# Performance work log

Hardware: AMD Instinct MI355X
Metric: run time of the kernel (lower is better)

The kernel has to match this reference:

```python
import jax, jax.numpy as jnp
import numpy as np

B, T, D, H = 4, 2048, 1024, 16
DH = D // H

def setup_inputs() -> dict:
    key = jax.random.key(0)
    ks = jax.random.split(key, 8)
    scale = 1.0 / np.sqrt(D)
    return {
        "q": jax.random.normal(ks[0], (B, T, D), dtype=jnp.float32),
        "k": jax.random.normal(ks[1], (B, T, D), dtype=jnp.float32),
        "v": jax.random.normal(ks[2], (B, T, D), dtype=jnp.float32),
        "wq": jax.random.normal(ks[3], (D, D), dtype=jnp.float32) * scale,
        "wk": jax.random.normal(ks[4], (D, D), dtype=jnp.float32) * scale,
        "wv": jax.random.normal(ks[5], (D, D), dtype=jnp.float32) * scale,
        "wo": jax.random.normal(ks[6], (D, D), dtype=jnp.float32) * scale,
        "mask": jnp.tril(jnp.ones((T, T), dtype=bool)),  # causal [Tq,Tk]
    }

def reference(q, k, v, wq, wk, wv, wo, mask):
    Bq, Tq, C = q.shape
    Tk = k.shape[1]
    # nn.Linear(bias=False): y = x @ W.T, W is [out,in]
    qh = (q @ wq.T).reshape(Bq, Tq, H, DH).transpose(0, 2, 1, 3)  # [B,H,Tq,DH]
    kh = (k @ wk.T).reshape(Bq, Tk, H, DH).transpose(0, 2, 1, 3)
    vh = (v @ wv.T).reshape(Bq, Tk, H, DH).transpose(0, 2, 1, 3)
    att = jnp.einsum("bhqd,bhkd->bhqk", qh, kh) / np.sqrt(DH)
    att = jnp.where(mask[None, None, :, :], att, -jnp.inf)
    att = jax.nn.softmax(att, axis=-1)
    out = jnp.einsum("bhqk,bhkd->bhqd", att, vh)
    out = out.transpose(0, 2, 1, 3).reshape(Bq, Tq, C)
    return out @ wo.T
```

## Files before the change

### kernel.cpp

```cpp
#include <hip/hip_runtime.h>
#include <hip/hip_bf16.h>

typedef short bf16x8 __attribute__((ext_vector_type(8)));
typedef float f32x4 __attribute__((ext_vector_type(4)));
typedef float f32x16 __attribute__((ext_vector_type(16)));
typedef unsigned u32x2 __attribute__((ext_vector_type(2)));

#define N_B 4
#define N_T 2048
#define N_D 1024
#define N_H 16
#define N_DH 64

#define Q_SCALE 0.18033688011112042f

__device__ __forceinline__ unsigned short f2bf(float f) {
  union { float f; unsigned int u; } c; c.f = f;
  unsigned int u = c.u;
  return (unsigned short)((u + 0x7FFFu + ((u >> 16) & 1u)) >> 16);
}

__device__ __forceinline__ unsigned cvtpk_bf16(float lo, float hi) {
  unsigned r;
  asm("v_cvt_pk_bf16_f32 %0, %1, %2" : "=v"(r) : "v"(lo), "v"(hi));
  return r;
}

__device__ __forceinline__ void gll16(const unsigned short* g, unsigned short* l) {
  __builtin_amdgcn_global_load_lds(
      (const __attribute__((address_space(1))) unsigned int*)(const void*)g,
      (__attribute__((address_space(3))) unsigned int*)(void*)l, 16, 0, 0);
}

__global__ void cast_all(const float* __restrict__ wq, const float* __restrict__ wk,
                         const float* __restrict__ wv, const float* __restrict__ wo,
                         const float* __restrict__ q, const float* __restrict__ k,
                         const float* __restrict__ v,
                         unsigned short* __restrict__ ws) {
  const int z = blockIdx.z;
  const float* srcs[7] = {wq, wk, wv, wo, q, k, v};
  const int size = (z < 4) ? (N_D * N_D) : (N_B * N_T * N_D);
  const size_t off = (z < 4) ? (size_t)z * (N_D * N_D)
                             : (size_t)4 * (N_D * N_D) + (size_t)(z - 4) * (N_B * N_T * N_D);
  const int i = (blockIdx.x * 256 + threadIdx.x) * 8;
  if (i >= size) return;
  const float* src = srcs[z];
  float4 a = *(const float4*)(src + i);
  float4 b = *(const float4*)(src + i + 4);
  bf16x8 p;
  p[0] = (short)f2bf(a.x); p[1] = (short)f2bf(a.y);
  p[2] = (short)f2bf(a.z); p[3] = (short)f2bf(a.w);
  p[4] = (short)f2bf(b.x); p[5] = (short)f2bf(b.y);
  p[6] = (short)f2bf(b.z); p[7] = (short)f2bf(b.w);
  *(bf16x8*)(ws + off + i) = p;
}

__launch_bounds__(256, 2)
__global__ void proj_qkv(const unsigned short* __restrict__ qb,
                         const unsigned short* __restrict__ kb,
                         const unsigned short* __restrict__ vb,
                         const unsigned short* __restrict__ wq,
                         const unsigned short* __restrict__ wk,
                         const unsigned short* __restrict__ wv,
                         unsigned short* __restrict__ qh,
                         unsigned short* __restrict__ kh,
                         unsigned short* __restrict__ vt) {
  const int z = blockIdx.z;
  const unsigned short* X = (z == 0) ? qb : (z == 1) ? kb : vb;
  const unsigned short* W = (z == 0) ? wq : (z == 1) ? wk : wv;
  unsigned short* O = (z == 0) ? qh : (z == 1) ? kh : vt;

  __shared__ unsigned short lds_a[128 * 64];
  __shared__ unsigned short lds_b[128 * 64];

  const int tid = threadIdx.x;
  const int wave = tid >> 6, lane = tid & 63;
  const int wm = wave >> 1, wn = wave & 1;
  const int lr = lane & 15, lg = lane >> 4;
  const int orig = blockIdx.y * 8 + blockIdx.x;
  const int swz = (orig & 7) * 64 + (orig >> 3);
  const int m0 = (swz >> 3) * 128, n0 = (swz & 7) * 128;
  const int sw = (lr & 7) << 4;

  f32x4 acc[4][4] = {};

  for (int k0 = 0; k0 < N_D; k0 += 64) {
    __syncthreads();
#pragma unroll
    for (int it = 0; it < 4; ++it) {
      int c = it * 256 + tid;
      int row = c >> 3;
      int sb = ((c & 7) * 16) ^ ((row & 7) << 4);
      gll16(&X[(size_t)(m0 + row) * N_D + k0 + (sb >> 1)], &lds_a[c * 8]);
      gll16(&W[(size_t)(n0 + row) * N_D + k0 + (sb >> 1)], &lds_b[c * 8]);
    }
    __syncthreads();

#pragma unroll
    for (int kk = 0; kk < 2; ++kk) {
      bf16x8 af[4], bfr[4];
      const int cb = (lg * 16 + kk * 64);
#pragma unroll
      for (int m = 0; m < 4; ++m)
        af[m] = *(bf16x8*)&lds_a[(wm * 64 + m * 16 + lr) * 64 + ((cb ^ sw) >> 1)];
#pragma unroll
      for (int n = 0; n < 4; ++n)
        bfr[n] = *(bf16x8*)&lds_b[(wn * 64 + n * 16 + lr) * 64 + ((cb ^ sw) >> 1)];
#pragma unroll
      for (int m = 0; m < 4; ++m)
#pragma unroll
        for (int n = 0; n < 4; ++n)
          acc[m][n] = __builtin_amdgcn_mfma_f32_16x16x32_bf16(af[m], bfr[n], acc[m][n], 0, 0, 0);
    }
  }

  const float osc = (z == 0) ? Q_SCALE : 1.0f;
#pragma unroll
  for (int m = 0; m < 4; ++m)
#pragma unroll
    for (int n = 0; n < 4; ++n)
#pragma unroll
      for (int r = 0; r < 4; ++r) {
        int row = m0 + wm * 64 + m * 16 + lg * 4 + r;
        int col = n0 + wn * 64 + n * 16 + lr;
        int b = row >> 11, t = row & (N_T - 1);
        int hh = col >> 6, dh = col & 63;
        unsigned short val = f2bf(acc[m][n][r] * osc);
        if (z < 2)
          O[(((size_t)(b * N_H + hh)) * N_T + t) * N_DH + dh] = val;
        else
          O[(((size_t)(b * N_H + hh)) * N_DH + dh) * N_T + t] = val;
      }
}

__launch_bounds__(256, 2)
__global__ void proj_out(const unsigned short* __restrict__ A,
                         const unsigned short* __restrict__ W,
                         float* __restrict__ out) {
  __shared__ unsigned short lds_a[128 * 64];
  __shared__ unsigned short lds_b[128 * 64];

  const int tid = threadIdx.x;
  const int wave = tid >> 6, lane = tid & 63;
  const int wm = wave >> 1, wn = wave & 1;
  const int lr = lane & 15, lg = lane >> 4;
  const int orig = blockIdx.y * 8 + blockIdx.x;
  const int swz = (orig & 7) * 64 + (orig >> 3);
  const int m0 = (swz >> 3) * 128, n0 = (swz & 7) * 128;
  const int sw = (lr & 7) << 4;

  f32x4 acc[4][4] = {};

  for (int k0 = 0; k0 < N_D; k0 += 64) {
    __syncthreads();
#pragma unroll
    for (int it = 0; it < 4; ++it) {
      int c = it * 256 + tid;
      int row = c >> 3;
      int sb = ((c & 7) * 16) ^ ((row & 7) << 4);
      gll16(&A[(size_t)(m0 + row) * N_D + k0 + (sb >> 1)], &lds_a[c * 8]);
      gll16(&W[(size_t)(n0 + row) * N_D + k0 + (sb >> 1)], &lds_b[c * 8]);
    }
    __syncthreads();

#pragma unroll
    for (int kk = 0; kk < 2; ++kk) {
      bf16x8 af[4], bfr[4];
      const int cb = (lg * 16 + kk * 64);
#pragma unroll
      for (int m = 0; m < 4; ++m)
        af[m] = *(bf16x8*)&lds_a[(wm * 64 + m * 16 + lr) * 64 + ((cb ^ sw) >> 1)];
#pragma unroll
      for (int n = 0; n < 4; ++n)
        bfr[n] = *(bf16x8*)&lds_b[(wn * 64 + n * 16 + lr) * 64 + ((cb ^ sw) >> 1)];
#pragma unroll
      for (int m = 0; m < 4; ++m)
#pragma unroll
        for (int n = 0; n < 4; ++n)
          acc[m][n] = __builtin_amdgcn_mfma_f32_16x16x32_bf16(af[m], bfr[n], acc[m][n], 0, 0, 0);
    }
  }

#pragma unroll
  for (int m = 0; m < 4; ++m)
#pragma unroll
    for (int n = 0; n < 4; ++n)
#pragma unroll
      for (int r = 0; r < 4; ++r) {
        int row = m0 + wm * 64 + m * 16 + lg * 4 + r;
        int col = n0 + wn * 64 + n * 16 + lr;
        out[(size_t)row * N_D + col] = acc[m][n][r];
      }
}

__launch_bounds__(256, 2)
__global__ void attn(const unsigned short* __restrict__ qh,
                     const unsigned short* __restrict__ kh,
                     const unsigned short* __restrict__ vt,
                     unsigned short* __restrict__ att) {
  __shared__ unsigned short k_lds[2][64 * 64];
  __shared__ unsigned short v_lds[2][64 * 64];

  const int tid = threadIdx.x;
  const int wave = tid >> 6, lane = tid & 63;
  const int l31 = lane & 31, hi = lane >> 5;
  const int L = (int)blockIdx.x + (int)blockIdx.y * 8;
  const int bh = (L & 7) | ((L >> 6) << 3);
  const int px = (L >> 3) & 7;
  const size_t base = (size_t)bh * N_T * N_DH;
  const unsigned short* Q = qh + base;
  const unsigned short* K = kh + base;
  const unsigned short* V = vt + base;
  const int b = bh >> 4, h = bh & 15;
  const int swr = (l31 & 7) << 4;

  bf16x8 ones;
#pragma unroll
  for (int j = 0; j < 8; ++j) ones[j] = (short)0x3F80;

  auto stage = [&](int buf, int kb2) {
    const int kk0 = kb2 * 64;
#pragma unroll
    for (int it = 0; it < 2; ++it) {
      int c = it * 256 + tid;
      int row = c >> 3;
      int sb = ((c & 7) * 16) ^ ((row & 7) << 4);
      gll16(&K[(size_t)(kk0 + row) * N_DH + (sb >> 1)], &k_lds[buf][c * 8]);
      gll16(&V[(size_t)row * N_T + kk0 + (sb >> 1)], &v_lds[buf][c * 8]);
    }
  };

  for (int half = 0; half < 2; ++half) {
    const int qt = half ? (15 - px) : px;
    const int q0w = qt * 128 + wave * 32;

    bf16x8 qf[4];
#pragma unroll
    for (int i = 0; i < 4; ++i)
      qf[i] = *(const bf16x8*)&Q[(size_t)(q0w + l31) * N_DH + i * 16 + hi * 8];

    float m_r = -INFINITY;
    f32x16 l_acc = {};
    f32x16 o0 = {}, o1 = {};

    const int nkb = 2 * qt + 2;

    __syncthreads();
    stage(0, 0);

    for (int kb = 0; kb < nkb; ++kb) {
      const int cur = kb & 1;
      __syncthreads();
      if (kb + 1 < nkb) stage(cur ^ 1, kb + 1);

      const unsigned short* kt_ = k_lds[cur];
      const unsigned short* vt_ = v_lds[cur];

      const int kgb0 = kb * 64;
      const int kgb1 = kb * 64 + 32;
      if (kgb0 > q0w + 31) continue;
      const bool a1 = (kgb1 <= q0w + 31);

      f32x16 s0 = {}, s1 = {};
      __builtin_amdgcn_s_setprio(1);
#pragma unroll
      for (int i = 0; i < 4; ++i) {
        bf16x8 kf = *(const bf16x8*)&kt_[l31 * 64 + (((i * 32 + hi * 16) ^ swr) >> 1)];
        s0 = __builtin_amdgcn_mfma_f32_32x32x16_bf16(kf, qf[i], s0, 0, 0, 0);
      }
      if (a1) {
#pragma unroll
        for (int i = 0; i < 4; ++i) {
          bf16x8 kf = *(const bf16x8*)&kt_[(32 + l31) * 64 + (((i * 32 + hi * 16) ^ swr) >> 1)];
          s1 = __builtin_amdgcn_mfma_f32_32x32x16_bf16(kf, qf[i], s1, 0, 0, 0);
        }
      }
      __builtin_amdgcn_s_setprio(0);

      if (kgb0 == q0w) {
#pragma unroll
        for (int j = 0; j < 16; ++j)
          if ((j & 3) + 8 * (j >> 2) + 4 * hi > l31) s0[j] = -1e30f;
      }
      if (a1 && kgb1 == q0w) {
#pragma unroll
        for (int j = 0; j < 16; ++j)
          if ((j & 3) + 8 * (j >> 2) + 4 * hi > l31) s1[j] = -1e30f;
      }

      float mx = s0[0];
#pragma unroll
      for (int j = 1; j < 16; ++j) mx = fmaxf(mx, s0[j]);
      if (a1) {
#pragma unroll
        for (int j = 0; j < 16; ++j) mx = fmaxf(mx, s1[j]);
      }
      {
        u32x2 rm = __builtin_amdgcn_permlane32_swap(
            __float_as_uint(mx), __float_as_uint(mx), false, false);
        mx = fmaxf(__uint_as_float(rm.x), __uint_as_float(rm.y));
      }
      if (__any(mx > m_r + 8.0f)) {
        float mn = fmaxf(m_r, mx);
        float al = exp2f(m_r - mn);
        m_r = mn;
#pragma unroll
        for (int j = 0; j < 16; ++j) {
          float aj = __shfl(al, (j & 3) + 8 * (j >> 2) + 4 * hi);
          o0[j] *= aj; o1[j] *= aj; l_acc[j] *= aj;
        }
      }

#pragma unroll
      for (int j = 0; j < 16; ++j) s0[j] = exp2f(s0[j] - m_r);
      if (a1) {
#pragma unroll
        for (int j = 0; j < 16; ++j) s1[j] = exp2f(s1[j] - m_r);
      }

      {
        unsigned t01 = cvtpk_bf16(s0[0], s0[1]),   t45 = cvtpk_bf16(s0[4], s0[5]);
        unsigned t23 = cvtpk_bf16(s0[2], s0[3]),   t67 = cvtpk_bf16(s0[6], s0[7]);
        unsigned u01 = cvtpk_bf16(s0[8], s0[9]),   u45 = cvtpk_bf16(s0[12], s0[13]);
        unsigned u23 = cvtpk_bf16(s0[10], s0[11]), u67 = cvtpk_bf16(s0[14], s0[15]);
        u32x2 r0 = __builtin_amdgcn_permlane32_swap(t01, t45, false, false);
        u32x2 r1 = __builtin_amdgcn_permlane32_swap(t23, t67, false, false);
        u32x2 r2 = __builtin_amdgcn_permlane32_swap(u01, u45, false, false);
        u32x2 r3 = __builtin_amdgcn_permlane32_swap(u23, u67, false, false);
        union { unsigned u[4]; bf16x8 v; } pa0, pa1;
        pa0.u[0] = r0.x;  pa0.u[1] = r1.x;  pa0.u[2] = r0.y;  pa0.u[3] = r1.y;
        pa1.u[0] = r2.x;  pa1.u[1] = r3.x;  pa1.u[2] = r2.y;  pa1.u[3] = r3.y;

        const int c0 = ((hi * 16) ^ swr) >> 1;
        const int c1 = ((32 + hi * 16) ^ swr) >> 1;
        bf16x8 v00 = *(const bf16x8*)&vt_[l31 * 64 + c0];
        bf16x8 v01 = *(const bf16x8*)&vt_[(32 + l31) * 64 + c0];
        bf16x8 v10 = *(const bf16x8*)&vt_[l31 * 64 + c1];
        bf16x8 v11 = *(const bf16x8*)&vt_[(32 + l31) * 64 + c1];

        __builtin_amdgcn_s_setprio(1);
        o0 = __builtin_amdgcn_mfma_f32_32x32x16_bf16(pa0.v, v00, o0, 0, 0, 0);
        o1 = __builtin_amdgcn_mfma_f32_32x32x16_bf16(pa0.v, v01, o1, 0, 0, 0);
        o0 = __builtin_amdgcn_mfma_f32_32x32x16_bf16(pa1.v, v10, o0, 0, 0, 0);
        o1 = __builtin_amdgcn_mfma_f32_32x32x16_bf16(pa1.v, v11, o1, 0, 0, 0);
        l_acc = __builtin_amdgcn_mfma_f32_32x32x16_bf16(pa0.v, ones, l_acc, 0, 0, 0);
        l_acc = __builtin_amdgcn_mfma_f32_32x32x16_bf16(pa1.v, ones, l_acc, 0, 0, 0);
        __builtin_amdgcn_s_setprio(0);
      }

      if (a1) {
        unsigned t01 = cvtpk_bf16(s1[0], s1[1]),   t45 = cvtpk_bf16(s1[4], s1[5]);
        unsigned t23 = cvtpk_bf16(s1[2], s1[3]),   t67 = cvtpk_bf16(s1[6], s1[7]);
        unsigned u01 = cvtpk_bf16(s1[8], s1[9]),   u45 = cvtpk_bf16(s1[12], s1[13]);
        unsigned u23 = cvtpk_bf16(s1[10], s1[11]), u67 = cvtpk_bf16(s1[14], s1[15]);
        u32x2 r0 = __builtin_amdgcn_permlane32_swap(t01, t45, false, false);
        u32x2 r1 = __builtin_amdgcn_permlane32_swap(t23, t67, false, false);
        u32x2 r2 = __builtin_amdgcn_permlane32_swap(u01, u45, false, false);
        u32x2 r3 = __builtin_amdgcn_permlane32_swap(u23, u67, false, false);
        union { unsigned u[4]; bf16x8 v; } pb0, pb1;
        pb0.u[0] = r0.x;  pb0.u[1] = r1.x;  pb0.u[2] = r0.y;  pb0.u[3] = r1.y;
        pb1.u[0] = r2.x;  pb1.u[1] = r3.x;  pb1.u[2] = r2.y;  pb1.u[3] = r3.y;

        const int c0 = ((64 + hi * 16) ^ swr) >> 1;
        const int c1 = ((96 + hi * 16) ^ swr) >> 1;
        bf16x8 v00 = *(const bf16x8*)&vt_[l31 * 64 + c0];
        bf16x8 v01 = *(const bf16x8*)&vt_[(32 + l31) * 64 + c0];
        bf16x8 v10 = *(const bf16x8*)&vt_[l31 * 64 + c1];
        bf16x8 v11 = *(const bf16x8*)&vt_[(32 + l31) * 64 + c1];

        __builtin_amdgcn_s_setprio(1);
        o0 = __builtin_amdgcn_mfma_f32_32x32x16_bf16(pb0.v, v00, o0, 0, 0, 0);
        o1 = __builtin_amdgcn_mfma_f32_32x32x16_bf16(pb0.v, v01, o1, 0, 0, 0);
        o0 = __builtin_amdgcn_mfma_f32_32x32x16_bf16(pb1.v, v10, o0, 0, 0, 0);
        o1 = __builtin_amdgcn_mfma_f32_32x32x16_bf16(pb1.v, v11, o1, 0, 0, 0);
        l_acc = __builtin_amdgcn_mfma_f32_32x32x16_bf16(pb0.v, ones, l_acc, 0, 0, 0);
        l_acc = __builtin_amdgcn_mfma_f32_32x32x16_bf16(pb1.v, ones, l_acc, 0, 0, 0);
        __builtin_amdgcn_s_setprio(0);
      }
    }

#pragma unroll
    for (int j = 0; j < 16; ++j) {
      float inv = 1.0f / l_acc[j];
      int t = q0w + (j & 3) + 8 * (j >> 2) + 4 * hi;
      size_t rowb = ((size_t)(b * N_T + t)) * N_D + h * 64 + l31;
      att[rowb]      = f2bf(o0[j] * inv);
      att[rowb + 32] = f2bf(o1[j] * inv);
    }
  }
}

extern "C" void kernel_launch(void* const* d_in, const int* in_sizes, int n_in,
                              void* d_out, int out_size, void* d_ws, size_t ws_size,
                              hipStream_t stream) {
  (void)in_sizes; (void)n_in; (void)out_size; (void)ws_size;
  const float* q  = (const float*)d_in[0];
  const float* k  = (const float*)d_in[1];
  const float* v  = (const float*)d_in[2];
  const float* wq = (const float*)d_in[3];
  const float* wk = (const float*)d_in[4];
  const float* wv = (const float*)d_in[5];
  const float* wo = (const float*)d_in[6];
  float* out = (float*)d_out;

  unsigned short* ws = (unsigned short*)d_ws;
  const size_t W_ELEMS = (size_t)N_D * N_D;
  const size_t T_ELEMS = (size_t)N_B * N_T * N_D;
  unsigned short* wqb = ws;
  unsigned short* wkb = wqb + W_ELEMS;
  unsigned short* wvb = wkb + W_ELEMS;
  unsigned short* wob = wvb + W_ELEMS;
  unsigned short* qb  = wob + W_ELEMS;
  unsigned short* kb  = qb + T_ELEMS;
  unsigned short* vb  = kb + T_ELEMS;
  unsigned short* qhb = vb + T_ELEMS;
  unsigned short* khb = qhb + T_ELEMS;
  unsigned short* vtb = khb + T_ELEMS;
  unsigned short* att = qb;

  cast_all<<<dim3(4096, 1, 7), 256, 0, stream>>>(wq, wk, wv, wo, q, k, v, ws);
  proj_qkv<<<dim3(8, 64, 3), 256, 0, stream>>>(qb, kb, vb, wqb, wkb, wvb, qhb, khb, vtb);
  attn<<<dim3(8, N_B * N_H), 256, 0, stream>>>(qhb, khb, vtb, att);
  proj_out<<<dim3(8, 64), 256, 0, stream>>>(att, wob, out);
}
```

Measured before the change: 194.8 us.

## Split attention over two KV halves and merge partials in a combine kernel

The attention kernel now launches twice as many blocks, and each one handles half of the key/value range for its query tiles. Each block writes normalized partial outputs plus per-row max and sum to workspace. A new combine kernel rescales and merges the two partials into the final attention output. This aims to raise parallelism and occupancy (launch bounds raised to 4 blocks per CU), at the cost of an extra kernel launch, extra global traffic, and bf16 rounding of the partial outputs.

New measurement: 220.4 us. +13.2%, slower.

```diff
diff --git a/kernel.cpp b/kernel.cpp
--- a/kernel.cpp
+++ b/kernel.cpp
@@ -11,6 +11,7 @@
 #define N_D 1024
 #define N_H 16
 #define N_DH 64
+#define N_ROWS (N_B * N_H * N_T)
 
 #define Q_SCALE 0.18033688011112042f
 
@@ -193,25 +194,28 @@
       }
 }
 
-__launch_bounds__(256, 2)
+__launch_bounds__(256, 4)
 __global__ void attn(const unsigned short* __restrict__ qh,
-                     const unsigned short* __restrict__ kh,
+                     const unsigned short* __restrict__ kh_,
                      const unsigned short* __restrict__ vt,
-                     unsigned short* __restrict__ att) {
+                     unsigned short* __restrict__ oP0,
+                     unsigned short* __restrict__ oP1,
+                     float* __restrict__ mlP) {
   __shared__ unsigned short k_lds[2][64 * 64];
   __shared__ unsigned short v_lds[2][64 * 64];
 
   const int tid = threadIdx.x;
   const int wave = tid >> 6, lane = tid & 63;
   const int l31 = lane & 31, hi = lane >> 5;
-  const int L = (int)blockIdx.x + (int)blockIdx.y * 8;
-  const int bh = (L & 7) | ((L >> 6) << 3);
-  const int px = (L >> 3) & 7;
+  const int L = (int)blockIdx.x + (int)blockIdx.y * 16;
+  const int bh = (L & 7) | (((L >> 3) & 7) << 3);
+  const int top = L >> 6;
+  const int px = top >> 1;
+  const int khalf = top & 1;
   const size_t base = (size_t)bh * N_T * N_DH;
   const unsigned short* Q = qh + base;
-  const unsigned short* K = kh + base;
+  const unsigned short* K = kh_ + base;
   const unsigned short* V = vt + base;
-  const int b = bh >> 4, h = bh & 15;
   const int swr = (l31 & 7) << 4;
 
   bf16x8 ones;
@@ -230,8 +234,10 @@
     }
   };
 
-  for (int half = 0; half < 2; ++half) {
-    const int qt = half ? (15 - px) : px;
+  for (int pass = 0; pass < 2; ++pass) {
+    const int qt = pass ? px : (15 - px);
+    const int s0 = khalf * (qt + 1);
+    const int s1 = s0 + (qt + 1);
     const int q0w = qt * 128 + wave * 32;
 
     bf16x8 qf[4];
@@ -239,19 +245,17 @@
     for (int i = 0; i < 4; ++i)
       qf[i] = *(const bf16x8*)&Q[(size_t)(q0w + l31) * N_DH + i * 16 + hi * 8];
 
-    float m_r = -INFINITY;
+    float m_r = -1e30f;
     f32x16 l_acc = {};
     f32x16 o0 = {}, o1 = {};
 
-    const int nkb = 2 * qt + 2;
-
     __syncthreads();
-    stage(0, 0);
-
-    for (int kb = 0; kb < nkb; ++kb) {
-      const int cur = kb & 1;
+    stage(0, s0);
+
+    for (int kb = s0; kb < s1; ++kb) {
+      const int cur = (kb - s0) & 1;
       __syncthreads();
-      if (kb + 1 < nkb) stage(cur ^ 1, kb + 1);
+      if (kb + 1 < s1) stage(cur ^ 1, kb + 1);
 
       const unsigned short* kt_ = k_lds[cur];
       const unsigned short* vt_ = v_lds[cur];
@@ -261,18 +265,18 @@
       if (kgb0 > q0w + 31) continue;
       const bool a1 = (kgb1 <= q0w + 31);
 
-      f32x16 s0 = {}, s1 = {};
+      f32x16 s0v = {}, s1v = {};
       __builtin_amdgcn_s_setprio(1);
 #pragma unroll
       for (int i = 0; i < 4; ++i) {
         bf16x8 kf = *(const bf16x8*)&kt_[l31 * 64 + (((i * 32 + hi * 16) ^ swr) >> 1)];
-        s0 = __builtin_amdgcn_mfma_f32_32x32x16_bf16(kf, qf[i], s0, 0, 0, 0);
+        s0v = __builtin_amdgcn_mfma_f32_32x32x16_bf16(kf, qf[i], s0v, 0, 0, 0);
       }
       if (a1) {
 #pragma unroll
         for (int i = 0; i < 4; ++i) {
           bf16x8 kf = *(const bf16x8*)&kt_[(32 + l31) * 64 + (((i * 32 + hi * 16) ^ swr) >> 1)];
-          s1 = __builtin_amdgcn_mfma_f32_32x32x16_bf16(kf, qf[i], s1, 0, 0, 0);
+          s1v = __builtin_amdgcn_mfma_f32_32x32x16_bf16(kf, qf[i], s1v, 0, 0, 0);
         }
       }
       __builtin_amdgcn_s_setprio(0);
@@ -280,20 +284,20 @@
       if (kgb0 == q0w) {
 #pragma unroll
         for (int j = 0; j < 16; ++j)
-          if ((j & 3) + 8 * (j >> 2) + 4 * hi > l31) s0[j] = -1e30f;
+          if ((j & 3) + 8 * (j >> 2) + 4 * hi > l31) s0v[j] = -1e30f;
       }
       if (a1 && kgb1 == q0w) {
 #pragma unroll
         for (int j = 0; j < 16; ++j)
-          if ((j & 3) + 8 * (j >> 2) + 4 * hi > l31) s1[j] = -1e30f;
-      }
-
-      float mx = s0[0];
-#pragma unroll
-      for (int j = 1; j < 16; ++j) mx = fmaxf(mx, s0[j]);
+          if ((j & 3) + 8 * (j >> 2) + 4 * hi > l31) s1v[j] = -1e30f;
+      }
+
+      float mx = s0v[0];
+#pragma unroll
+      for (int j = 1; j < 16; ++j) mx = fmaxf(mx, s0v[j]);
       if (a1) {
 #pragma unroll
-        for (int j = 0; j < 16; ++j) mx = fmaxf(mx, s1[j]);
+        for (int j = 0; j < 16; ++j) mx = fmaxf(mx, s1v[j]);
       }
       {
         u32x2 rm = __builtin_amdgcn_permlane32_swap(
@@ -312,17 +316,17 @@
       }
 
 #pragma unroll
-      for (int j = 0; j < 16; ++j) s0[j] = exp2f(s0[j] - m_r);
+      for (int j = 0; j < 16; ++j) s0v[j] = exp2f(s0v[j] - m_r);
       if (a1) {
 #pragma unroll
-        for (int j = 0; j < 16; ++j) s1[j] = exp2f(s1[j] - m_r);
+        for (int j = 0; j < 16; ++j) s1v[j] = exp2f(s1v[j] - m_r);
       }
 
       {
-        unsigned t01 = cvtpk_bf16(s0[0], s0[1]),   t45 = cvtpk_bf16(s0[4], s0[5]);
-        unsigned t23 = cvtpk_bf16(s0[2], s0[3]),   t67 = cvtpk_bf16(s0[6], s0[7]);
-        unsigned u01 = cvtpk_bf16(s0[8], s0[9]),   u45 = cvtpk_bf16(s0[12], s0[13]);
-        unsigned u23 = cvtpk_bf16(s0[10], s0[11]), u67 = cvtpk_bf16(s0[14], s0[15]);
+        unsigned t01 = cvtpk_bf16(s0v[0], s0v[1]),   t45 = cvtpk_bf16(s0v[4], s0v[5]);
+        unsigned t23 = cvtpk_bf16(s0v[2], s0v[3]),   t67 = cvtpk_bf16(s0v[6], s0v[7]);
+        unsigned u01 = cvtpk_bf16(s0v[8], s0v[9]),   u45 = cvtpk_bf16(s0v[12], s0v[13]);
+        unsigned u23 = cvtpk_bf16(s0v[10], s0v[11]), u67 = cvtpk_bf16(s0v[14], s0v[15]);
         u32x2 r0 = __builtin_amdgcn_permlane32_swap(t01, t45, false, false);
         u32x2 r1 = __builtin_amdgcn_permlane32_swap(t23, t67, false, false);
         u32x2 r2 = __builtin_amdgcn_permlane32_swap(u01, u45, false, false);
@@ -349,10 +353,10 @@
       }
 
       if (a1) {
-        unsigned t01 = cvtpk_bf16(s1[0], s1[1]),   t45 = cvtpk_bf16(s1[4], s1[5]);
-        unsigned t23 = cvtpk_bf16(s1[2], s1[3]),   t67 = cvtpk_bf16(s1[6], s1[7]);
-        unsigned u01 = cvtpk_bf16(s1[8], s1[9]),   u45 = cvtpk_bf16(s1[12], s1[13]);
-        unsigned u23 = cvtpk_bf16(s1[10], s1[11]), u67 = cvtpk_bf16(s1[14], s1[15]);
+        unsigned t01 = cvtpk_bf16(s1v[0], s1v[1]),   t45 = cvtpk_bf16(s1v[4], s1v[5]);
+        unsigned t23 = cvtpk_bf16(s1v[2], s1v[3]),   t67 = cvtpk_bf16(s1v[6], s1v[7]);
+        unsigned u01 = cvtpk_bf16(s1v[8], s1v[9]),   u45 = cvtpk_bf16(s1v[12], s1v[13]);
+        unsigned u23 = cvtpk_bf16(s1v[10], s1v[11]), u67 = cvtpk_bf16(s1v[14], s1v[15]);
         u32x2 r0 = __builtin_amdgcn_permlane32_swap(t01, t45, false, false);
         u32x2 r1 = __builtin_amdgcn_permlane32_swap(t23, t67, false, false);
         u32x2 r2 = __builtin_amdgcn_permlane32_swap(u01, u45, false, false);
@@ -379,15 +383,57 @@
       }
     }
 
+    unsigned short* oP = khalf ? oP1 : oP0;
+    float* mP = mlP + khalf * (2 * N_ROWS);
+    float* lP = mP + N_ROWS;
+    const int row0 = bh * N_T + q0w;
 #pragma unroll
     for (int j = 0; j < 16; ++j) {
-      float inv = 1.0f / l_acc[j];
-      int t = q0w + (j & 3) + 8 * (j >> 2) + 4 * hi;
-      size_t rowb = ((size_t)(b * N_T + t)) * N_D + h * 64 + l31;
-      att[rowb]      = f2bf(o0[j] * inv);
-      att[rowb + 32] = f2bf(o1[j] * inv);
-    }
+      float lv = l_acc[j];
+      float inv = lv > 0.f ? 1.0f / lv : 0.f;
+      int ridx = (j & 3) + 8 * (j >> 2) + 4 * hi;
+      size_t rb = (size_t)(row0 + ridx) * 64 + l31;
+      oP[rb]      = f2bf(o0[j] * inv);
+      oP[rb + 32] = f2bf(o1[j] * inv);
+    }
+    if (l31 == 0) {
+#pragma unroll
+      for (int j = 0; j < 16; ++j) {
+        int ridx = (j & 3) + 8 * (j >> 2) + 4 * hi;
+        lP[row0 + ridx] = l_acc[j];
+      }
+    }
+    if (hi == 0) mP[row0 + l31] = m_r;
   }
+}
+
+__global__ void combine(const unsigned short* __restrict__ oP0,
+                        const unsigned short* __restrict__ oP1,
+                        const float* __restrict__ mlP,
+                        unsigned short* __restrict__ att) {
+  const int gid = blockIdx.x * 256 + threadIdx.x;
+  const int row = gid >> 3;
+  const int dv0 = (gid & 7) * 8;
+  const float m1 = mlP[row],               l1 = mlP[N_ROWS + row];
+  const float m2 = mlP[2 * N_ROWS + row],  l2 = mlP[3 * N_ROWS + row];
+  const float mm = fmaxf(m1, m2);
+  const float w1 = exp2f(m1 - mm) * l1;
+  const float w2 = exp2f(m2 - mm) * l2;
+  const float inv = 1.0f / (w1 + w2);
+  const float c1 = w1 * inv, c2 = w2 * inv;
+  bf16x8 a = *(const bf16x8*)&oP0[(size_t)row * 64 + dv0];
+  bf16x8 bvv = *(const bf16x8*)&oP1[(size_t)row * 64 + dv0];
+  const int bh = row >> 11, t = row & (N_T - 1);
+  const int b = bh >> 4, h = bh & 15;
+  unsigned short* dst = att + ((size_t)(b * N_T + t)) * N_D + h * 64 + dv0;
+  bf16x8 r;
+#pragma unroll
+  for (int i = 0; i < 8; ++i) {
+    float f1 = __uint_as_float(((unsigned)(unsigned short)a[i]) << 16);
+    float f2 = __uint_as_float(((unsigned)(unsigned short)bvv[i]) << 16);
+    r[i] = (short)f2bf(f1 * c1 + f2 * c2);
+  }
+  *(bf16x8*)dst = r;
 }
 
 extern "C" void kernel_launch(void* const* d_in, const int* in_sizes, int n_in,
@@ -417,9 +463,13 @@
   unsigned short* khb = qhb + T_ELEMS;
   unsigned short* vtb = khb + T_ELEMS;
   unsigned short* att = qb;
+  unsigned short* oP0 = kb;
+  unsigned short* oP1 = vb;
+  float* mlP = (float*)(vtb + T_ELEMS);
 
   cast_all<<<dim3(4096, 1, 7), 256, 0, stream>>>(wq, wk, wv, wo, q, k, v, ws);
   proj_qkv<<<dim3(8, 64, 3), 256, 0, stream>>>(qb, kb, vb, wqb, wkb, wvb, qhb, khb, vtb);
-  attn<<<dim3(8, N_B * N_H), 256, 0, stream>>>(qhb, khb, vtb, att);
+  attn<<<dim3(16, 64), 256, 0, stream>>>(qhb, khb, vtb, oP0, oP1, mlP);
+  combine<<<dim3(4096), 256, 0, stream>>>(oP0, oP1, mlP, att);
   proj_out<<<dim3(8, 64), 256, 0, stream>>>(att, wob, out);
 }
```
